# Performance work log

Hardware: AMD Instinct MI355X
Metric: run time of the kernel (lower is better)

## Reference

```python
import jax, jax.numpy as jnp
import numpy as np

I = 1024
H = 1024
B = 4096
EPS = 1e-5

def layer_norm(x, gamma, beta):
    mu = jnp.mean(x, axis=-1, keepdims=True)
    var = jnp.var(x, axis=-1, keepdims=True)
    return (x - mu) * jax.lax.rsqrt(var + EPS) * gamma + beta

def setup_inputs() -> dict:
    key = jax.random.key(0)
    ks = jax.random.split(key, 5)
    return {
        "input": jax.random.normal(ks[0], (B, I), dtype=jnp.float32),
        "hx": jax.random.normal(ks[1], (B, H), dtype=jnp.float32),
        "cx": jax.random.normal(ks[2], (B, H), dtype=jnp.float32),
        "weight_ih": jax.random.normal(ks[3], (4 * H, I), dtype=jnp.float32),
        "weight_hh": jax.random.normal(ks[4], (4 * H, H), dtype=jnp.float32),
        "gamma_i": jnp.ones((4 * H,), jnp.float32),
        "beta_i": jnp.zeros((4 * H,), jnp.float32),
        "gamma_h": jnp.ones((4 * H,), jnp.float32),
        "beta_h": jnp.zeros((4 * H,), jnp.float32),
        "gamma_c": jnp.ones((H,), jnp.float32),
        "beta_c": jnp.zeros((H,), jnp.float32),
    }

def reference(input, hx, cx, weight_ih, weight_hh,
              gamma_i, beta_i, gamma_h, beta_h, gamma_c, beta_c):
    # igates: [B, 4H]
    igates = layer_norm(jnp.dot(input, weight_ih.T), gamma_i, beta_i)
    hgates = layer_norm(jnp.dot(hx, weight_hh.T), gamma_h, beta_h)
    gates = igates + hgates
    ingate, forgetgate, cellgate, outgate = jnp.split(gates, 4, axis=1)
    ingate = jax.nn.sigmoid(ingate)
    forgetgate = jax.nn.sigmoid(forgetgate)
    cellgate = jnp.tanh(cellgate)
    outgate = jax.nn.sigmoid(outgate)
    cy = layer_norm(forgetgate * cx + ingate * cellgate, gamma_c, beta_c)
    hy = outgate * jnp.tanh(cy)
    return (hy, hy, cy)
```

## Files before the change

### kernel.cpp

```cpp
#include <hip/hip_runtime.h>

#define EPS 1e-5f

typedef unsigned short u16;
typedef __attribute__((ext_vector_type(8))) __bf16 bf16x8;
typedef __attribute__((ext_vector_type(4))) float f32x4;
typedef __attribute__((ext_vector_type(8))) unsigned short ushort8;

__device__ inline float bf2f(u16 h) {
  union { unsigned u; float f; } x; x.u = ((unsigned)h) << 16; return x.f;
}
__device__ inline u16 f2bf(float f) {
  union { float f; unsigned u; } x; x.f = f;
  unsigned r = x.u + 0x7fffu + ((x.u >> 16) & 1u);
  return (u16)(r >> 16);
}
__device__ inline float sigmoidf(float x) { return 1.0f / (1.0f + __expf(-x)); }

__global__ __launch_bounds__(256) void cast4_f32_bf16(
    const float* __restrict__ s0, const float* __restrict__ s1,
    const float* __restrict__ s2, const float* __restrict__ s3,
    u16* __restrict__ d0, u16* __restrict__ d1,
    u16* __restrict__ d2, u16* __restrict__ d3, int n)
{
  const float* s = (blockIdx.y == 0) ? s0 : (blockIdx.y == 1) ? s1 : (blockIdx.y == 2) ? s2 : s3;
  u16*         d = (blockIdx.y == 0) ? d0 : (blockIdx.y == 1) ? d1 : (blockIdx.y == 2) ? d2 : d3;
  int i = (blockIdx.x * 256 + threadIdx.x) * 8;
  if (i >= n) return;
  float4 a = *(const float4*)(s + i);
  float4 b = *(const float4*)(s + i + 4);
  ushort8 o;
  o[0] = f2bf(a.x); o[1] = f2bf(a.y); o[2] = f2bf(a.z); o[3] = f2bf(a.w);
  o[4] = f2bf(b.x); o[5] = f2bf(b.y); o[6] = f2bf(b.z); o[7] = f2bf(b.w);
  *(ushort8*)(d + i) = o;
}

#define MFMA_ __builtin_amdgcn_mfma_f32_16x16x32_bf16
#define ASG __attribute__((address_space(1)))
#define ASL __attribute__((address_space(3)))

#define GLL(p, lds) __builtin_amdgcn_global_load_lds( \
    (const ASG void*)(p), (ASL void*)(lds), 16, 0, 0);

#define STAGE(nx, kn) \
  GLL(gA_0 + (kn), &sA[nx][(      tid) * 8]) \
  GLL(gA_1 + (kn), &sA[nx][(256 + tid) * 8]) \
  GLL(gB_0 + (kn), &sB[nx][(      tid) * 8]) \
  GLL(gB_1 + (kn), &sB[nx][(256 + tid) * 8])

#define LDA(mi) (*(const bf16x8*)&sa[(arow + (mi) * 16) * 32 + rslot])
#define LDB(ni) (*(const bf16x8*)&sb[(brow + (ni) * 16) * 32 + rslot])

#define VMW(n) asm volatile("s_waitcnt vmcnt(" #n ")" ::: "memory");
#define BAR __builtin_amdgcn_s_barrier();

#define MFMA16 \
  acc[0][0] = MFMA_(a0, b0, acc[0][0], 0, 0, 0); \
  acc[0][1] = MFMA_(a0, b1, acc[0][1], 0, 0, 0); \
  acc[0][2] = MFMA_(a0, b2, acc[0][2], 0, 0, 0); \
  acc[0][3] = MFMA_(a0, b3, acc[0][3], 0, 0, 0); \
  acc[1][0] = MFMA_(a1, b0, acc[1][0], 0, 0, 0); \
  acc[1][1] = MFMA_(a1, b1, acc[1][1], 0, 0, 0); \
  acc[1][2] = MFMA_(a1, b2, acc[1][2], 0, 0, 0); \
  acc[1][3] = MFMA_(a1, b3, acc[1][3], 0, 0, 0); \
  acc[2][0] = MFMA_(a2, b0, acc[2][0], 0, 0, 0); \
  acc[2][1] = MFMA_(a2, b1, acc[2][1], 0, 0, 0); \
  acc[2][2] = MFMA_(a2, b2, acc[2][2], 0, 0, 0); \
  acc[2][3] = MFMA_(a2, b3, acc[2][3], 0, 0, 0); \
  acc[3][0] = MFMA_(a3, b0, acc[3][0], 0, 0, 0); \
  acc[3][1] = MFMA_(a3, b1, acc[3][1], 0, 0, 0); \
  acc[3][2] = MFMA_(a3, b2, acc[3][2], 0, 0, 0); \
  acc[3][3] = MFMA_(a3, b3, acc[3][3], 0, 0, 0);

__global__ __launch_bounds__(256, 4) void gemm128_dual(
    const u16* __restrict__ A0, const u16* __restrict__ W0, u16* __restrict__ C0,
    const u16* __restrict__ A1, const u16* __restrict__ W1, u16* __restrict__ C1)
{
  constexpr int K = 1024, N = 4096, NT = 32;

  __shared__ __attribute__((aligned(16))) u16 sA[2][128 * 32];
  __shared__ __attribute__((aligned(16))) u16 sB[2][128 * 32];

  const int bid = blockIdx.x;
  const u16* A  = (bid < 1024) ? A0 : A1;
  const u16* Wm = (bid < 1024) ? W0 : W1;
  u16*       C  = (bid < 1024) ? C0 : C1;
  const int b2 = bid & 1023;
  const int bm = (b2 >> 5) << 7;
  const int bn = (b2 & 31) << 7;

  const int tid = threadIdx.x;
  const int l  = tid & 63;
  const int w  = tid >> 6;
  const int wr = w >> 1;
  const int wc = w & 1;

  const int srow = tid >> 2;
  const int scol = ((tid & 3) ^ ((tid >> 3) & 3)) * 8;
  const u16* gA_0 = A  + (size_t)(bm + srow) * K + scol;
  const u16* gA_1 = gA_0 + (size_t)64 * K;
  const u16* gB_0 = Wm + (size_t)(bn + srow) * K + scol;
  const u16* gB_1 = gB_0 + (size_t)64 * K;

  const int arow = wr * 64 + (l & 15);
  const int brow = wc * 64 + (l & 15);
  const int rslot = ((l >> 4) ^ ((l >> 1) & 3)) * 8;

  f32x4 acc[4][4];
#pragma unroll
  for (int i = 0; i < 4; ++i)
#pragma unroll
    for (int j = 0; j < 4; ++j) acc[i][j] = (f32x4){0.f, 0.f, 0.f, 0.f};

  STAGE(0, 0)

  for (int t = 0; t < NT; ++t) {
    const int cur = t & 1, nxt = cur ^ 1;
    const u16* sa = sA[cur];
    const u16* sb = sB[cur];

    if (t < NT - 1) {
      STAGE(nxt, (t + 1) * 32)
      VMW(4)
    } else {
      VMW(0)
    }
    BAR

    bf16x8 a0, a1, a2, a3, b0, b1, b2, b3;
    b0 = LDB(0); b1 = LDB(1); b2 = LDB(2); b3 = LDB(3);
    a0 = LDA(0); a1 = LDA(1); a2 = LDA(2); a3 = LDA(3);
    MFMA16

    BAR
  }

  const int ccol = bn + wc * 64 + (l & 15);
  const int crow = bm + wr * 64 + (l >> 4) * 4;
#pragma unroll
  for (int mi = 0; mi < 4; ++mi) {
#pragma unroll
    for (int ni = 0; ni < 4; ++ni) {
      int col = ccol + ni * 16;
#pragma unroll
      for (int r = 0; r < 4; ++r) {
        int row = crow + mi * 16 + r;
        C[(size_t)row * N + col] = f2bf(acc[mi][ni][r]);
      }
    }
  }
}

__global__ __launch_bounds__(256) void lstm_epilogue(
    const u16* __restrict__ ig, const u16* __restrict__ hg,
    const float* __restrict__ cx,
    const float* __restrict__ gi, const float* __restrict__ bi,
    const float* __restrict__ gh, const float* __restrict__ bh,
    const float* __restrict__ gc, const float* __restrict__ bc,
    float* __restrict__ out)
{
  const int b = blockIdx.x;
  const int t = threadIdx.x;
  const u16* igr = ig + (size_t)b * 4096;
  const u16* hgr = hg + (size_t)b * 4096;

  __shared__ float redbuf[16];

  float iv[16], hv[16];
  float s_i = 0.f, q_i = 0.f, s_h = 0.f, q_h = 0.f;
#pragma unroll
  for (int i = 0; i < 16; ++i) {
    float a = bf2f(igr[t + 256 * i]);
    float c = bf2f(hgr[t + 256 * i]);
    iv[i] = a; hv[i] = c;
    s_i += a; q_i += a * a; s_h += c; q_h += c * c;
  }
#pragma unroll
  for (int off = 32; off > 0; off >>= 1) {
    s_i += __shfl_xor(s_i, off);
    q_i += __shfl_xor(q_i, off);
    s_h += __shfl_xor(s_h, off);
    q_h += __shfl_xor(q_h, off);
  }
  {
    int wv = t >> 6;
    if ((t & 63) == 0) {
      redbuf[wv] = s_i; redbuf[wv + 4] = q_i;
      redbuf[wv + 8] = s_h; redbuf[wv + 12] = q_h;
    }
    __syncthreads();
    s_i = redbuf[0] + redbuf[1] + redbuf[2] + redbuf[3];
    q_i = redbuf[4] + redbuf[5] + redbuf[6] + redbuf[7];
    s_h = redbuf[8] + redbuf[9] + redbuf[10] + redbuf[11];
    q_h = redbuf[12] + redbuf[13] + redbuf[14] + redbuf[15];
    __syncthreads();
  }
  const float inv4096 = 1.0f / 4096.0f;
  float mu_i = s_i * inv4096;
  float rs_i = rsqrtf(q_i * inv4096 - mu_i * mu_i + EPS);
  float mu_h = s_h * inv4096;
  float rs_h = rsqrtf(q_h * inv4096 - mu_h * mu_h + EPS);

  float c_pre[4], og[4];
  float s_c = 0.f, q_c = 0.f;
#pragma unroll
  for (int i = 0; i < 4; ++i) {
    int h = t + 256 * i;
    float g_in = ((iv[i]      - mu_i) * rs_i * gi[h]        + bi[h]) +
                 ((hv[i]      - mu_h) * rs_h * gh[h]        + bh[h]);
    float g_fg = ((iv[i + 4]  - mu_i) * rs_i * gi[h + 1024] + bi[h + 1024]) +
                 ((hv[i + 4]  - mu_h) * rs_h * gh[h + 1024] + bh[h + 1024]);
    float g_cl = ((iv[i + 8]  - mu_i) * rs_i * gi[h + 2048] + bi[h + 2048]) +
                 ((hv[i + 8]  - mu_h) * rs_h * gh[h + 2048] + bh[h + 2048]);
    float g_og = ((iv[i + 12] - mu_i) * rs_i * gi[h + 3072] + bi[h + 3072]) +
                 ((hv[i + 12] - mu_h) * rs_h * gh[h + 3072] + bh[h + 3072]);
    float in_s = sigmoidf(g_in);
    float fg_s = sigmoidf(g_fg);
    float cl_t = tanhf(g_cl);
    og[i] = sigmoidf(g_og);
    c_pre[i] = fg_s * cx[(size_t)b * 1024 + h] + in_s * cl_t;
    s_c += c_pre[i]; q_c += c_pre[i] * c_pre[i];
  }
#pragma unroll
  for (int off = 32; off > 0; off >>= 1) {
    s_c += __shfl_xor(s_c, off);
    q_c += __shfl_xor(q_c, off);
  }
  {
    int wv = t >> 6;
    if ((t & 63) == 0) { redbuf[wv] = s_c; redbuf[wv + 4] = q_c; }
    __syncthreads();
    s_c = redbuf[0] + redbuf[1] + redbuf[2] + redbuf[3];
    q_c = redbuf[4] + redbuf[5] + redbuf[6] + redbuf[7];
  }
  const float inv1024 = 1.0f / 1024.0f;
  float mu_c = s_c * inv1024;
  float rs_c = rsqrtf(q_c * inv1024 - mu_c * mu_c + EPS);

  const size_t BH = (size_t)4096 * 1024;
#pragma unroll
  for (int i = 0; i < 4; ++i) {
    int h = t + 256 * i;
    float cy = (c_pre[i] - mu_c) * rs_c * gc[h] + bc[h];
    float hy = og[i] * tanhf(cy);
    size_t o = (size_t)b * 1024 + h;
    out[o] = hy;
    out[BH + o] = hy;
    out[2 * BH + o] = cy;
  }
}

extern "C" void kernel_launch(void* const* d_in, const int* in_sizes, int n_in,
                              void* d_out, int out_size, void* d_ws, size_t ws_size,
                              hipStream_t stream) {
  const float* input = (const float*)d_in[0];
  const float* hx    = (const float*)d_in[1];
  const float* cx    = (const float*)d_in[2];
  const float* wih   = (const float*)d_in[3];
  const float* whh   = (const float*)d_in[4];
  const float* gi    = (const float*)d_in[5];
  const float* bi    = (const float*)d_in[6];
  const float* gh    = (const float*)d_in[7];
  const float* bh    = (const float*)d_in[8];
  const float* gc    = (const float*)d_in[9];
  const float* bc    = (const float*)d_in[10];
  float* out = (float*)d_out;

  char* wsp = (char*)d_ws;
  u16* a_bf  = (u16*)(wsp);
  u16* h_bf  = (u16*)(wsp + ((size_t)8  << 20));
  u16* wi_bf = (u16*)(wsp + ((size_t)16 << 20));
  u16* wh_bf = (u16*)(wsp + ((size_t)24 << 20));
  u16* ig_bf = (u16*)(wsp + ((size_t)32 << 20));
  u16* hg_bf = (u16*)(wsp + ((size_t)64 << 20));

  const int nper = 4096 * 1024;
  dim3 cgrid(nper / 8 / 256, 4);
  cast4_f32_bf16<<<cgrid, 256, 0, stream>>>(input, hx, wih, whh,
                                            a_bf, h_bf, wi_bf, wh_bf, nper);

  gemm128_dual<<<2048, 256, 0, stream>>>(a_bf, wi_bf, ig_bf,
                                         h_bf, wh_bf, hg_bf);

  lstm_epilogue<<<4096, 256, 0, stream>>>(ig_bf, hg_bf, cx,
                                          gi, bi, gh, bh, gc, bc, out);
}
```

Measured before the change: 132.1 us.

## Use 256x128 GEMM tiles with 32x32x16 MFMA and XCD-aware block remap

Measured after the change: 127.6 us. -3.4%, faster.

```diff
diff --git a/kernel.cpp b/kernel.cpp
--- a/kernel.cpp
+++ b/kernel.cpp
@@ -4,7 +4,7 @@
 
 typedef unsigned short u16;
 typedef __attribute__((ext_vector_type(8))) __bf16 bf16x8;
-typedef __attribute__((ext_vector_type(4))) float f32x4;
+typedef __attribute__((ext_vector_type(16))) float f32x16;
 typedef __attribute__((ext_vector_type(8))) unsigned short ushort8;
 
 __device__ inline float bf2f(u16 h) {
@@ -35,7 +35,7 @@
   *(ushort8*)(d + i) = o;
 }
 
-#define MFMA_ __builtin_amdgcn_mfma_f32_16x16x32_bf16
+#define MFMA32x32_ __builtin_amdgcn_mfma_f32_32x32x16_bf16
 #define ASG __attribute__((address_space(1)))
 #define ASL __attribute__((address_space(3)))
 
@@ -44,49 +44,38 @@
 
 #define STAGE(nx, kn) \
   GLL(gA_0 + (kn), &sA[nx][(      tid) * 8]) \
-  GLL(gA_1 + (kn), &sA[nx][(256 + tid) * 8]) \
-  GLL(gB_0 + (kn), &sB[nx][(      tid) * 8]) \
-  GLL(gB_1 + (kn), &sB[nx][(256 + tid) * 8])
-
-#define LDA(mi) (*(const bf16x8*)&sa[(arow + (mi) * 16) * 32 + rslot])
-#define LDB(ni) (*(const bf16x8*)&sb[(brow + (ni) * 16) * 32 + rslot])
+  GLL(gA_1 + (kn), &sA[nx][(512 + tid) * 8]) \
+  GLL(gB_0 + (kn), &sB[nx][(      tid) * 8])
+
+#define LDA(mi, sl) (*(const bf16x8*)&sa[(arow + (mi) * 32) * 32 + (sl)])
+#define LDB(nj, sl) (*(const bf16x8*)&sb[(brow + (nj) * 32) * 32 + (sl)])
 
 #define VMW(n) asm volatile("s_waitcnt vmcnt(" #n ")" ::: "memory");
 #define BAR __builtin_amdgcn_s_barrier();
 
-#define MFMA16 \
-  acc[0][0] = MFMA_(a0, b0, acc[0][0], 0, 0, 0); \
-  acc[0][1] = MFMA_(a0, b1, acc[0][1], 0, 0, 0); \
-  acc[0][2] = MFMA_(a0, b2, acc[0][2], 0, 0, 0); \
-  acc[0][3] = MFMA_(a0, b3, acc[0][3], 0, 0, 0); \
-  acc[1][0] = MFMA_(a1, b0, acc[1][0], 0, 0, 0); \
-  acc[1][1] = MFMA_(a1, b1, acc[1][1], 0, 0, 0); \
-  acc[1][2] = MFMA_(a1, b2, acc[1][2], 0, 0, 0); \
-  acc[1][3] = MFMA_(a1, b3, acc[1][3], 0, 0, 0); \
-  acc[2][0] = MFMA_(a2, b0, acc[2][0], 0, 0, 0); \
-  acc[2][1] = MFMA_(a2, b1, acc[2][1], 0, 0, 0); \
-  acc[2][2] = MFMA_(a2, b2, acc[2][2], 0, 0, 0); \
-  acc[2][3] = MFMA_(a2, b3, acc[2][3], 0, 0, 0); \
-  acc[3][0] = MFMA_(a3, b0, acc[3][0], 0, 0, 0); \
-  acc[3][1] = MFMA_(a3, b1, acc[3][1], 0, 0, 0); \
-  acc[3][2] = MFMA_(a3, b2, acc[3][2], 0, 0, 0); \
-  acc[3][3] = MFMA_(a3, b3, acc[3][3], 0, 0, 0);
-
-__global__ __launch_bounds__(256, 4) void gemm128_dual(
+#define MFMA4(aa0, aa1, bb0, bb1) \
+  acc[0][0] = MFMA32x32_(aa0, bb0, acc[0][0], 0, 0, 0); \
+  acc[0][1] = MFMA32x32_(aa0, bb1, acc[0][1], 0, 0, 0); \
+  acc[1][0] = MFMA32x32_(aa1, bb0, acc[1][0], 0, 0, 0); \
+  acc[1][1] = MFMA32x32_(aa1, bb1, acc[1][1], 0, 0, 0);
+
+__global__ __launch_bounds__(512, 4) void gemm256x128_dual(
     const u16* __restrict__ A0, const u16* __restrict__ W0, u16* __restrict__ C0,
     const u16* __restrict__ A1, const u16* __restrict__ W1, u16* __restrict__ C1)
 {
   constexpr int K = 1024, N = 4096, NT = 32;
 
-  __shared__ __attribute__((aligned(16))) u16 sA[2][128 * 32];
+  __shared__ __attribute__((aligned(16))) u16 sA[2][256 * 32];
   __shared__ __attribute__((aligned(16))) u16 sB[2][128 * 32];
 
-  const int bid = blockIdx.x;
-  const u16* A  = (bid < 1024) ? A0 : A1;
-  const u16* Wm = (bid < 1024) ? W0 : W1;
-  u16*       C  = (bid < 1024) ? C0 : C1;
-  const int b2 = bid & 1023;
-  const int bm = (b2 >> 5) << 7;
+  const int b0_ = blockIdx.x;
+  const int bid = (b0_ & 7) * 128 + (b0_ >> 3);
+
+  const u16* A  = (bid < 512) ? A0 : A1;
+  const u16* Wm = (bid < 512) ? W0 : W1;
+  u16*       C  = (bid < 512) ? C0 : C1;
+  const int b2 = bid & 511;
+  const int bm = (b2 >> 5) << 8;
   const int bn = (b2 & 31) << 7;
 
   const int tid = threadIdx.x;
@@ -98,19 +87,23 @@
   const int srow = tid >> 2;
   const int scol = ((tid & 3) ^ ((tid >> 3) & 3)) * 8;
   const u16* gA_0 = A  + (size_t)(bm + srow) * K + scol;
-  const u16* gA_1 = gA_0 + (size_t)64 * K;
+  const u16* gA_1 = gA_0 + (size_t)128 * K;
   const u16* gB_0 = Wm + (size_t)(bn + srow) * K + scol;
-  const u16* gB_1 = gB_0 + (size_t)64 * K;
-
-  const int arow = wr * 64 + (l & 15);
-  const int brow = wc * 64 + (l & 15);
-  const int rslot = ((l >> 4) ^ ((l >> 1) & 3)) * 8;
-
-  f32x4 acc[4][4];
-#pragma unroll
-  for (int i = 0; i < 4; ++i)
-#pragma unroll
-    for (int j = 0; j < 4; ++j) acc[i][j] = (f32x4){0.f, 0.f, 0.f, 0.f};
+
+  const int arow = wr * 64 + (l & 31);
+  const int brow = wc * 64 + (l & 31);
+  const int g  = l >> 5;
+  const int xs = (l >> 1) & 3;
+  const int sl0 = ((0 + g) ^ xs) * 8;
+  const int sl1 = ((2 + g) ^ xs) * 8;
+
+  f32x16 acc[2][2];
+#pragma unroll
+  for (int i = 0; i < 2; ++i)
+#pragma unroll
+    for (int j = 0; j < 2; ++j)
+#pragma unroll
+      for (int r = 0; r < 16; ++r) acc[i][j][r] = 0.f;
 
   STAGE(0, 0)
 
@@ -121,31 +114,34 @@
 
     if (t < NT - 1) {
       STAGE(nxt, (t + 1) * 32)
-      VMW(4)
+      VMW(3)
     } else {
       VMW(0)
     }
     BAR
 
-    bf16x8 a0, a1, a2, a3, b0, b1, b2, b3;
-    b0 = LDB(0); b1 = LDB(1); b2 = LDB(2); b3 = LDB(3);
-    a0 = LDA(0); a1 = LDA(1); a2 = LDA(2); a3 = LDA(3);
-    MFMA16
+    bf16x8 a0e, a1e, a0o, a1o, b0e, b1e, b0o, b1o;
+    b0e = LDB(0, sl0); b1e = LDB(1, sl0);
+    b0o = LDB(0, sl1); b1o = LDB(1, sl1);
+    a0e = LDA(0, sl0); a1e = LDA(1, sl0);
+    a0o = LDA(0, sl1); a1o = LDA(1, sl1);
+    MFMA4(a0e, a1e, b0e, b1e)
+    MFMA4(a0o, a1o, b0o, b1o)
 
     BAR
   }
 
-  const int ccol = bn + wc * 64 + (l & 15);
-  const int crow = bm + wr * 64 + (l >> 4) * 4;
-#pragma unroll
-  for (int mi = 0; mi < 4; ++mi) {
-#pragma unroll
-    for (int ni = 0; ni < 4; ++ni) {
-      int col = ccol + ni * 16;
-#pragma unroll
-      for (int r = 0; r < 4; ++r) {
-        int row = crow + mi * 16 + r;
-        C[(size_t)row * N + col] = f2bf(acc[mi][ni][r]);
+  const int ccol = bn + wc * 64 + (l & 31);
+  const int crow = bm + wr * 64 + 4 * (l >> 5);
+#pragma unroll
+  for (int mi = 0; mi < 2; ++mi) {
+#pragma unroll
+    for (int nj = 0; nj < 2; ++nj) {
+      int col = ccol + nj * 32;
+#pragma unroll
+      for (int r = 0; r < 16; ++r) {
+        int row = crow + mi * 32 + (r & 3) + 8 * (r >> 2);
+        C[(size_t)row * N + col] = f2bf(acc[mi][nj][r]);
       }
     }
   }
@@ -279,8 +275,8 @@
   cast4_f32_bf16<<<cgrid, 256, 0, stream>>>(input, hx, wih, whh,
                                             a_bf, h_bf, wi_bf, wh_bf, nper);
 
-  gemm128_dual<<<2048, 256, 0, stream>>>(a_bf, wi_bf, ig_bf,
-                                         h_bf, wh_bf, hg_bf);
+  gemm256x128_dual<<<1024, 512, 0, stream>>>(a_bf, wi_bf, ig_bf,
+                                             h_bf, wh_bf, hg_bf);
 
   lstm_epilogue<<<4096, 256, 0, stream>>>(ig_bf, hg_bf, cx,
                                           gi, bi, gh, bh, gc, bc, out);
```
